# Kernel tuning notes

Hardware: AMD Instinct MI355X
Metric: run time of the kernel (lower is better)

The kernel has to match this reference:

```python
import jax, jax.numpy as jnp
import numpy as np

N_NODES = 51200      # 128 graphs * 400 ROIs
N_ROI = 400
HID = 64             # 'batch_size' arg of the torch module = hidden channels = n_timepoints
N_EDGES = 1638400    # avg degree 32
N_CLASSES = 2
NEG_SLOPE = 0.01


def setup_inputs():
    key = jax.random.key(0)
    ks = jax.random.split(key, 20)
    s = 0.05
    inp = {
        'x': jax.random.normal(ks[0], (N_NODES, HID), dtype=jnp.float32),
        'edge_index': jax.random.randint(ks[1], (2, N_EDGES), 0, N_NODES, dtype=jnp.int64),
        'edge_weight': jax.random.uniform(ks[2], (N_EDGES,), dtype=jnp.float32),
        # GCNConv weights stored [in, out]; biases [out]
        'W1': jax.random.normal(ks[3], (HID, HID), dtype=jnp.float32) * s,
        'b1': jnp.zeros((HID,), jnp.float32),
        'W2': jax.random.normal(ks[4], (HID, HID), dtype=jnp.float32) * s,
        'b2': jnp.zeros((HID,), jnp.float32),
        'W3': jax.random.normal(ks[5], (HID, HID), dtype=jnp.float32) * s,
        'b3': jnp.zeros((HID,), jnp.float32),
        'W4': jax.random.normal(ks[6], (HID, HID), dtype=jnp.float32) * s,
        'b4': jnp.zeros((HID,), jnp.float32),
        'fc1_w': jax.random.normal(ks[7], (N_ROI * HID, 256), dtype=jnp.float32) * 0.01,
        'fc1_b': jnp.zeros((256,), jnp.float32),
        'fc2_w': jax.random.normal(ks[8], (256, 128), dtype=jnp.float32) * s,
        'fc2_b': jnp.zeros((128,), jnp.float32),
        'fc3_w': jax.random.normal(ks[9], (128, N_CLASSES), dtype=jnp.float32) * s,
        'fc3_b': jnp.zeros((N_CLASSES,), jnp.float32),
    }
    return inp


def _gcn_norm(edge_index, edge_weight, n):
    # PyG GCNConv: add self-loops (weight 1), symmetric D^-1/2 A D^-1/2 normalization
    loop = jnp.arange(n, dtype=edge_index.dtype)
    src = jnp.concatenate([edge_index[0], loop])
    dst = jnp.concatenate([edge_index[1], loop])
    w = jnp.concatenate([edge_weight, jnp.ones((n,), edge_weight.dtype)])
    deg = jax.ops.segment_sum(w, dst, num_segments=n)
    dis = jnp.where(deg > 0, jax.lax.rsqrt(jnp.maximum(deg, 1e-30)), 0.0)
    norm = dis[src] * w * dis[dst]
    return src, dst, norm


def _conv(h, W, b, src, dst, norm, n):
    h = h @ W                                   # [N, out]
    msg = h[src] * norm[:, None]                # gather + scale
    out = jax.ops.segment_sum(msg, dst, num_segments=n) + b
    return out


def _leaky(v):
    return jnp.where(v >= 0, v, NEG_SLOPE * v)


def _head(h, fc1_w, fc1_b, fc2_w, fc2_b, fc3_w, fc3_b):
    # global_mean_pool with batch = arange(N) is identity; pool == reshape to graphs
    g = h.reshape(-1, N_ROI * HID)              # [G, n_roi*hid]
    g = g @ fc1_w + fc1_b                       # dropout is eval-mode identity
    g = g @ fc2_w + fc2_b
    g = g @ fc3_w + fc3_b
    return g


def reference(x, edge_index, edge_weight, W1, b1, W2, b2, W3, b3, W4, b4,
              fc1_w, fc1_b, fc2_w, fc2_b, fc3_w, fc3_b):
    n = x.shape[0]
    src, dst, norm = _gcn_norm(edge_index, edge_weight, n)
    h = _leaky(_conv(x, W1, b1, src, dst, norm, n))
    h = _leaky(_conv(h, W2, b2, src, dst, norm, n))
    h = _leaky(_conv(h, W3, b3, src, dst, norm, n))
    h = _leaky(_conv(h, W4, b4, src, dst, norm, n))
    logits = _head(h, fc1_w, fc1_b, fc2_w, fc2_b, fc3_w, fc3_b)
    logits0 = _head(x, fc1_w, fc1_b, fc2_w, fc2_b, fc3_w, fc3_b)
    penal = 0.09 * logits.shape[0] / jnp.linalg.norm(logits - logits0)
    return logits, penal
```

## Files before the change

### kernel.cpp

```cpp
#include <hip/hip_runtime.h>
#include <cstddef>

#define N_NODES 51200
#define N_EDGES 1638400
#define HID 64
#define N_ROI 400
#define N_GRAPHS 128
#define KHEAD 25600
#define NEG_SLOPE 0.01f
#define CAP 80
#define NCHUNK 200
#define CHUNK 8192
#define NBIN 1024
#define BINSZ 50
#define LSTRIDE 81
#define NWC 400

typedef unsigned short u16;
typedef unsigned int u32;
typedef unsigned char u8;
typedef float f32x2 __attribute__((ext_vector_type(2)));

__device__ inline u16 f2bf(float f) {
    u32 u = __float_as_uint(f);
    u32 r = u + 0x7FFFu + ((u >> 16) & 1u);
    return (u16)(r >> 16);
}
__device__ inline float bf2f(u16 h) { return __uint_as_float(((u32)h) << 16); }

__device__ inline f32x2 dec8lo(u32 v) { return __builtin_amdgcn_cvt_pk_f32_fp8((int)v, false); }
__device__ inline f32x2 dec8hi(u32 v) { return __builtin_amdgcn_cvt_pk_f32_fp8((int)v, true); }
template <bool HI>
__device__ inline u32 enc8(float a, float b, u32 old) {
    return (u32)__builtin_amdgcn_cvt_pk_fp8_f32(a, b, (int)old, HI);
}
__device__ inline u32 pack4_fp8(float a, float b, float c, float d) {
    u32 w = enc8<false>(a, b, 0u);
    return enc8<true>(c, d, w);
}


__global__ __launch_bounds__(1024) void k1(const int* __restrict__ ei,
                                           const float* __restrict__ ew,
                                           uint2* __restrict__ chunkData,
                                           u32* __restrict__ offcnt,
                                           const float* __restrict__ x,
                                           u8* __restrict__ x8,
                                           const float* __restrict__ fc2w,
                                           const float* __restrict__ fc3w,
                                           const float* __restrict__ fc1b,
                                           const float* __restrict__ fc2b,
                                           const float* __restrict__ fc3b,
                                           float* __restrict__ fc23,
                                           float* __restrict__ bc,
                                           float* __restrict__ sq,
                                           int* __restrict__ done) {
    int bid = blockIdx.x, t = threadIdx.x;
    __shared__ u32 cnt[NBIN];
    __shared__ u32 cur[NBIN];
    __shared__ u32 wsum[16];
    __shared__ uint2 stag[CHUNK];
    __shared__ float t1[128];

    if (bid < NCHUNK) {
        cnt[t] = 0;
        __syncthreads();
        int base = bid * CHUNK;
        const int4* sp = reinterpret_cast<const int4*>(ei + base);
        const int4* dp = reinterpret_cast<const int4*>(ei + N_EDGES + base);
        const float4* wp = reinterpret_cast<const float4*>(ew + base);
        int4 sa = sp[2 * t], sb = sp[2 * t + 1];
        int4 da = dp[2 * t], db = dp[2 * t + 1];
        float4 wa = wp[2 * t], wb = wp[2 * t + 1];
        int ss[8] = {sa.x, sa.y, sa.z, sa.w, sb.x, sb.y, sb.z, sb.w};
        int dd[8] = {da.x, da.y, da.z, da.w, db.x, db.y, db.z, db.w};
        float wv[8] = {wa.x, wa.y, wa.z, wa.w, wb.x, wb.y, wb.z, wb.w};
        u32 lo[8]; int bin[8];
        #pragma unroll
        for (int i = 0; i < 8; i++) {
            int b = (int)((u32)dd[i] / BINSZ);
            bin[i] = b;
            lo[i] = (u32)ss[i] | ((u32)(dd[i] - b * BINSZ) << 16);
            atomicAdd(&cnt[b], 1u);
        }
        __syncthreads();
        int wave = t >> 6, lane = t & 63;
        u32 v = cnt[t], inc = v;
        #pragma unroll
        for (int d = 1; d < 64; d <<= 1) {
            u32 o = __shfl_up(inc, d, 64);
            if (lane >= d) inc += o;
        }
        if (lane == 63) wsum[wave] = inc;
        __syncthreads();
        if (t == 0) {
            u32 r = 0;
            #pragma unroll
            for (int i = 0; i < 16; i++) { u32 c = wsum[i]; wsum[i] = r; r += c; }
        }
        __syncthreads();
        u32 excl = inc - v + wsum[wave];
        cur[t] = excl;
        offcnt[(size_t)bid * NBIN + t] = excl | (v << 16);
        __syncthreads();
        #pragma unroll
        for (int i = 0; i < 8; i++) {
            u32 pos = atomicAdd(&cur[bin[i]], 1u);
            stag[pos] = make_uint2(lo[i], __float_as_uint(wv[i]));
        }
        __syncthreads();
        const uint4* sg4 = reinterpret_cast<const uint4*>(stag);
        uint4* out4 = reinterpret_cast<uint4*>(chunkData + (size_t)base);
        #pragma unroll
        for (int i = 0; i < 4; i++) out4[i * 1024 + t] = sg4[i * 1024 + t];
    } else if (bid < 400) {
        int idx = (bid - NCHUNK) * 1024 + t;
        const float4* xp = reinterpret_cast<const float4*>(x) + (size_t)idx * 4;
        float4 a = xp[0], b = xp[1], c = xp[2], d = xp[3];
        reinterpret_cast<uint4*>(x8)[idx] =
            make_uint4(pack4_fp8(a.x, a.y, a.z, a.w), pack4_fp8(b.x, b.y, b.z, b.w),
                       pack4_fp8(c.x, c.y, c.z, c.w), pack4_fp8(d.x, d.y, d.z, d.w));
    } else {
        if (t == 256) *sq = 0.f;
        if (t == 257) *done = 0;
        if (t < 256) {
            float s0 = 0.f, s1 = 0.f;
            const float* row = fc2w + t * 128;
            for (int j = 0; j < 128; j++) {
                float a = row[j];
                s0 += a * fc3w[2 * j];
                s1 += a * fc3w[2 * j + 1];
            }
            fc23[2 * t] = s0;
            fc23[2 * t + 1] = s1;
        }
        if (t < 128) {
            float s = fc2b[t];
            for (int k = 0; k < 256; k++) s += fc1b[k] * fc2w[k * 128 + t];
            t1[t] = s;
        }
        __syncthreads();
        if (t < 2) {
            float s = fc3b[t];
            for (int j = 0; j < 128; j++) s += t1[j] * fc3w[2 * j + t];
            bc[t] = s;
        }
    }
}


__global__ __launch_bounds__(256) void k1t(const u32* __restrict__ in,
                                           u32* __restrict__ outT) {
    __shared__ u32 tile[32][33];
    int bx = blockIdx.x & 31, cy = blockIdx.x >> 5;
    int b0 = bx * 32, c0 = cy * 32;
    int tx = threadIdx.x & 31, ty = threadIdx.x >> 5;
    for (int i = ty; i < 32; i += 8) {
        int c = c0 + i;
        if (c < NCHUNK) tile[i][tx] = in[(size_t)c * NBIN + b0 + tx];
    }
    __syncthreads();
    for (int i = ty; i < 32; i += 8) {
        int b = b0 + i;
        int c = c0 + tx;
        if (c < NCHUNK) outT[(size_t)b * NCHUNK + c] = tile[tx][i];
    }
}


__global__ __launch_bounds__(512) void k2(const uint2* __restrict__ chunkData,
                                          const u32* __restrict__ offcntT,
                                          u32* __restrict__ buck,
                                          int* __restrict__ cnts,
                                          float* __restrict__ dis,
                                          const float* __restrict__ fc1w,
                                          const float* __restrict__ fc23,
                                          float* __restrict__ Wc) {
    int bid = blockIdx.x, t = threadIdx.x;
    __shared__ u32 lbuck[BINSZ * LSTRIDE];
    __shared__ u32 lcnt[BINSZ];
    __shared__ float ldeg[BINSZ];
    __shared__ u32 oc[NCHUNK];

    if (bid < NBIN) {
        if (t < BINSZ) { lcnt[t] = 0; ldeg[t] = 0.f; }
        if (t < NCHUNK) oc[t] = offcntT[(size_t)bid * NCHUNK + t];
        __syncthreads();
        int w = t >> 6, lane = t & 63;
        int sBase = w * 25;
        for (int j = 0; j < 32; j += 8) {
            int so = j + (lane >> 3);
            int s = sBase + so;
            int i0 = lane & 7;
            int k = 0, off = 0;
            if (so < 25) {
                u32 o = oc[s];
                off = (int)(o & 0xffffu);
                k = (int)(o >> 16);
            }
            const uint2* cd = chunkData + (size_t)s * CHUNK + off;
            for (int i = i0; i < k; i += 8) {
                uint2 e = cd[i];
                u32 node = e.x >> 16;
                u32 src = e.x & 0xffffu;
                float ww = __uint_as_float(e.y);
                u32 pos = atomicAdd(&lcnt[node], 1u);
                if (pos < CAP - 1) lbuck[node * LSTRIDE + pos] = ((u32)f2bf(ww) << 16) | src;
                atomicAdd(&ldeg[node], ww);
            }
        }
        __syncthreads();
        int sg = t >> 5, ln = t & 31;
        for (int n = sg; n < BINSZ; n += 16) {
            int node = bid * BINSZ + n;
            int k = min((int)lcnt[n], CAP - 1);
            u32* dst = buck + (size_t)node * CAP;
            for (int i = ln; i < k; i += 32) dst[i] = lbuck[n * LSTRIDE + i];
            if (ln == 0) {
                float d = rsqrtf(1.f + ldeg[n]);
                dis[node] = d;
                cnts[node] = k + 1;
                dst[k] = ((u32)f2bf(d * d) << 16) | (u32)node;
            }
        }
    } else {
        float* f23 = (float*)lbuck;
        f23[t] = fc23[t];
        __syncthreads();
        const float2* f2p = reinterpret_cast<const float2*>(f23);
        int row = (bid - NBIN) * 64 + (t >> 3);
        int p = t & 7;
        const float4* rp = reinterpret_cast<const float4*>(fc1w + (size_t)row * 256 + p * 32);
        float s0 = 0.f, s1 = 0.f;
        #pragma unroll
        for (int i = 0; i < 8; i++) {
            float4 a = rp[i];
            int kb = p * 32 + i * 4;
            float2 w0 = f2p[kb], w1 = f2p[kb + 1], w2 = f2p[kb + 2], w3 = f2p[kb + 3];
            s0 += a.x * w0.x + a.y * w1.x + a.z * w2.x + a.w * w3.x;
            s1 += a.x * w0.y + a.y * w1.y + a.z * w2.y + a.w * w3.y;
        }
        #pragma unroll
        for (int off = 4; off; off >>= 1) {
            s0 += __shfl_down(s0, off, 8);
            s1 += __shfl_down(s1, off, 8);
        }
        if (p == 0) reinterpret_cast<float2*>(Wc)[row] = make_float2(s0, s1);
    }
}


template <bool BAKE>
__global__ __launch_bounds__(256) void k_layer(const u8* __restrict__ H8,
                                               u32* __restrict__ buck,
                                               const int* __restrict__ cnts,
                                               const float* __restrict__ dis,
                                               const float* __restrict__ W,
                                               const float* __restrict__ bias,
                                               u8* __restrict__ Hout) {
    __shared__ float Ws[64][64];
    __shared__ float ZsT[64][33];
    int t = threadIdx.x;
    int base = blockIdx.x * 32;

    #pragma unroll
    for (int i = 0; i < 4; i++) {
        int f = t + i * 256;
        int kk = f >> 4, c4 = f & 15;
        float4 wv = reinterpret_cast<const float4*>(W)[f];
        *reinterpret_cast<float4*>(&Ws[kk][c4 * 4]) = wv;
    }

    int grp = t >> 3, sub = t & 7;
    int node = base + grp;
    int k = cnts[node];
    u32* bk = buck + (size_t)node * CAP;

    if (BAKE) {
        float d = dis[node];
        for (int j = sub; j < k - 1; j += 8) {
            u32 e = bk[j];
            float val = bf2f((u16)(e >> 16)) * d * dis[e & 0xffffu];
            bk[j] = ((u32)f2bf(val) << 16) | (e & 0xffffu);
        }
    }

    const uint2* H64 = reinterpret_cast<const uint2*>(H8);
    float a0 = 0.f, a1 = 0.f, a2 = 0.f, a3 = 0.f;
    float a4 = 0.f, a5 = 0.f, a6 = 0.f, a7 = 0.f;
    for (int j0 = 0; j0 < k; j0 += 8) {
        int idx = j0 + sub;
        u32 pre = (idx < k) ? bk[idx] : 0u;
        #pragma unroll
        for (int i = 0; i < 8; i++) {
            u32 e = (u32)__shfl((int)pre, i, 8);
            float val = __uint_as_float(e & 0xffff0000u);
            u32 src = e & 0xffffu;
            uint2 r = H64[(size_t)src * 8 + sub];
            f32x2 l0 = dec8lo(r.x), h0 = dec8hi(r.x);
            f32x2 l1 = dec8lo(r.y), h1 = dec8hi(r.y);
            a0 += val * l0.x; a1 += val * l0.y; a2 += val * h0.x; a3 += val * h0.y;
            a4 += val * l1.x; a5 += val * l1.y; a6 += val * h1.x; a7 += val * h1.y;
        }
    }
    ZsT[8 * sub + 0][grp] = a0; ZsT[8 * sub + 1][grp] = a1;
    ZsT[8 * sub + 2][grp] = a2; ZsT[8 * sub + 3][grp] = a3;
    ZsT[8 * sub + 4][grp] = a4; ZsT[8 * sub + 5][grp] = a5;
    ZsT[8 * sub + 6][grp] = a6; ZsT[8 * sub + 7][grp] = a7;
    __syncthreads();

    int rp2 = t >> 4, c4i = t & 15;
    int r0 = rp2 * 2, c0 = c4i * 4;
    float4 acc0 = {0,0,0,0}, acc1 = {0,0,0,0};
    #pragma unroll 8
    for (int kk = 0; kk < 64; kk++) {
        float z0 = ZsT[kk][r0];
        float z1 = ZsT[kk][r0 + 1];
        float4 w = *reinterpret_cast<const float4*>(&Ws[kk][c0]);
        acc0.x += z0 * w.x; acc0.y += z0 * w.y; acc0.z += z0 * w.z; acc0.w += z0 * w.w;
        acc1.x += z1 * w.x; acc1.y += z1 * w.y; acc1.z += z1 * w.z; acc1.w += z1 * w.w;
    }
    float4 bb = *reinterpret_cast<const float4*>(bias + c0);
    float v0 = acc0.x + bb.x, v1 = acc0.y + bb.y, v2 = acc0.z + bb.z, v3 = acc0.w + bb.w;
    float v4 = acc1.x + bb.x, v5 = acc1.y + bb.y, v6 = acc1.z + bb.z, v7 = acc1.w + bb.w;
    v0 = v0 >= 0.f ? v0 : NEG_SLOPE * v0;
    v1 = v1 >= 0.f ? v1 : NEG_SLOPE * v1;
    v2 = v2 >= 0.f ? v2 : NEG_SLOPE * v2;
    v3 = v3 >= 0.f ? v3 : NEG_SLOPE * v3;
    v4 = v4 >= 0.f ? v4 : NEG_SLOPE * v4;
    v5 = v5 >= 0.f ? v5 : NEG_SLOPE * v5;
    v6 = v6 >= 0.f ? v6 : NEG_SLOPE * v6;
    v7 = v7 >= 0.f ? v7 : NEG_SLOPE * v7;
    u32* outp = reinterpret_cast<u32*>(Hout);
    outp[(size_t)(base + r0) * 16 + c4i]     = pack4_fp8(v0, v1, v2, v3);
    outp[(size_t)(base + r0 + 1) * 16 + c4i] = pack4_fp8(v4, v5, v6, v7);
}


__global__ __launch_bounds__(256) void k_logits(const u8* __restrict__ h4,
                                                const u8* __restrict__ x8,
                                                const float* __restrict__ Wc,
                                                const float* __restrict__ bc,
                                                float* __restrict__ out,
                                                float* __restrict__ sq,
                                                int* __restrict__ done) {
    int g = blockIdx.x, t = threadIdx.x;
    const u8* bh = h4 + (size_t)g * KHEAD;
    const u8* bx = x8 + (size_t)g * KHEAD;
    float aH0 = 0.f, aH1 = 0.f, aX0 = 0.f, aX1 = 0.f;
    for (int k2 = t; k2 < KHEAD / 2; k2 += 256) {
        u32 hv = reinterpret_cast<const u16*>(bh)[k2];
        u32 xv = reinterpret_cast<const u16*>(bx)[k2];
        f32x2 h = dec8lo(hv);
        f32x2 xf = dec8lo(xv);
        float4 wc = reinterpret_cast<const float4*>(Wc)[k2];
        aH0 += h.x * wc.x + h.y * wc.z;
        aH1 += h.x * wc.y + h.y * wc.w;
        aX0 += xf.x * wc.x + xf.y * wc.z;
        aX1 += xf.x * wc.y + xf.y * wc.w;
    }
    for (int off = 32; off > 0; off >>= 1) {
        aH0 += __shfl_down(aH0, off);
        aH1 += __shfl_down(aH1, off);
        aX0 += __shfl_down(aX0, off);
        aX1 += __shfl_down(aX1, off);
    }
    __shared__ float red[4][4];
    int wave = t >> 6, lane = t & 63;
    if (lane == 0) {
        red[wave][0] = aH0; red[wave][1] = aH1;
        red[wave][2] = aX0; red[wave][3] = aX1;
    }
    __syncthreads();
    if (t == 0) {
        float h0 = red[0][0] + red[1][0] + red[2][0] + red[3][0];
        float h1 = red[0][1] + red[1][1] + red[2][1] + red[3][1];
        float x0 = red[0][2] + red[1][2] + red[2][2] + red[3][2];
        float x1 = red[0][3] + red[1][3] + red[2][3] + red[3][3];
        out[2 * g]     = h0 + bc[0];
        out[2 * g + 1] = h1 + bc[1];
        float d0 = h0 - x0, d1 = h1 - x1;
        atomicAdd(sq, d0 * d0 + d1 * d1);
        __threadfence();
        int c = atomicAdd(done, 1);
        if (c == N_GRAPHS - 1) {
            __threadfence();
            float s = atomicAdd(sq, 0.f);
            out[2 * N_GRAPHS] = 0.09f * (float)N_GRAPHS / sqrtf(s);
        }
    }
}


extern "C" void kernel_launch(void* const* d_in, const int* in_sizes, int n_in,
                              void* d_out, int out_size, void* d_ws, size_t ws_size,
                              hipStream_t stream) {
    const float* x    = (const float*)d_in[0];
    const int*   ei   = (const int*)d_in[1];
    const float* ew   = (const float*)d_in[2];
    const float* W1   = (const float*)d_in[3];
    const float* b1   = (const float*)d_in[4];
    const float* W2   = (const float*)d_in[5];
    const float* b2   = (const float*)d_in[6];
    const float* W3   = (const float*)d_in[7];
    const float* b3   = (const float*)d_in[8];
    const float* W4   = (const float*)d_in[9];
    const float* b4   = (const float*)d_in[10];
    const float* fc1w = (const float*)d_in[11];
    const float* fc1b = (const float*)d_in[12];
    const float* fc2w = (const float*)d_in[13];
    const float* fc2b = (const float*)d_in[14];
    const float* fc3w = (const float*)d_in[15];
    const float* fc3b = (const float*)d_in[16];
    float* out = (float*)d_out;

    char* base = (char*)d_ws;
    size_t off = 0;
    auto alloc = [&](size_t bytes) -> void* {
        void* p = base + off;
        off += (bytes + 255) & ~(size_t)255;
        return p;
    };
    uint2* chunkData = (uint2*)alloc((size_t)N_EDGES * 8);
    u32*   offcnt    = (u32*)alloc((size_t)NCHUNK * NBIN * 4);
    u32*   offcntT   = (u32*)alloc((size_t)NCHUNK * NBIN * 4);
    u32*   buck      = (u32*)alloc((size_t)N_NODES * CAP * 4);
    int*   cnts      = (int*)alloc((size_t)N_NODES * 4);
    float* dis       = (float*)alloc((size_t)N_NODES * 4);
    u8*    x8        = (u8*)alloc((size_t)N_NODES * HID);
    u8*    ha        = (u8*)alloc((size_t)N_NODES * HID);
    u8*    hb        = (u8*)alloc((size_t)N_NODES * HID);
    float* fc23      = (float*)alloc(512 * 4);
    float* bc        = (float*)alloc(2 * 4);
    float* Wc        = (float*)alloc((size_t)KHEAD * 2 * 4);
    char*  ctrl      = (char*)alloc(256);
    float* sq        = (float*)ctrl;
    int*   done      = (int*)(ctrl + 4);

    k1<<<401, 1024, 0, stream>>>(ei, ew, chunkData, offcnt, x, x8,
                                 fc2w, fc3w, fc1b, fc2b, fc3b, fc23, bc, sq, done);
    k1t<<<224, 256, 0, stream>>>(offcnt, offcntT);
    k2<<<NBIN + NWC, 512, 0, stream>>>(chunkData, offcntT, buck, cnts, dis,
                                       fc1w, fc23, Wc);

    const float* Wl[4] = {W1, W2, W3, W4};
    const float* bl[4] = {b1, b2, b3, b4};
    u8* hbufs[2] = {ha, hb};
    const u8* hin = x8;
    for (int l = 0; l < 4; l++) {
        u8* hout = hbufs[l & 1];
        if (l == 0)
            k_layer<true><<<N_NODES / 32, 256, 0, stream>>>(hin, buck, cnts, dis,
                                                            Wl[l], bl[l], hout);
        else
            k_layer<false><<<N_NODES / 32, 256, 0, stream>>>(hin, buck, cnts, dis,
                                                             Wl[l], bl[l], hout);
        hin = hout;
    }

    k_logits<<<N_GRAPHS, 256, 0, stream>>>(hin, x8, Wc, bc, out, sq, done);
}
```

Before: 163.8 us.

## Fuse logits head into last GCN layer and overlap x-logits with layer two

Removes the separate k_logits launch. The last layer now multiplies its leaky outputs directly by the collapsed head weights Wc and accumulates per-graph logits with atomics, so the final fp8 activation buffer is never stored or reread. A last-block-done counter finishes the output and the penalty norm. The x-side head dot products run as extra blocks appended to the layer-2 grid. This adds float atomics on per-graph accumulators, a second graph split inside blocks that straddle graphs, and a nondeterministic summation order.

```diff
diff --git a/kernel.cpp b/kernel.cpp
--- a/kernel.cpp
+++ b/kernel.cpp
@@ -15,6 +15,7 @@
 #define BINSZ 50
 #define LSTRIDE 81
 #define NWC 400
+#define NLB (N_NODES / 32)
 
 typedef unsigned short u16;
 typedef unsigned int u32;
@@ -53,7 +54,7 @@
                                            const float* __restrict__ fc3b,
                                            float* __restrict__ fc23,
                                            float* __restrict__ bc,
-                                           float* __restrict__ sq,
+                                           float* __restrict__ glog,
                                            int* __restrict__ done) {
     int bid = blockIdx.x, t = threadIdx.x;
     __shared__ u32 cnt[NBIN];
@@ -121,8 +122,8 @@
             make_uint4(pack4_fp8(a.x, a.y, a.z, a.w), pack4_fp8(b.x, b.y, b.z, b.w),
                        pack4_fp8(c.x, c.y, c.z, c.w), pack4_fp8(d.x, d.y, d.z, d.w));
     } else {
-        if (t == 256) *sq = 0.f;
-        if (t == 257) *done = 0;
+        if (t >= 256 && t < 512) glog[t - 256] = 0.f;
+        if (t == 512) *done = 0;
         if (t < 256) {
             float s0 = 0.f, s1 = 0.f;
             const float* row = fc2w + t * 128;
@@ -250,18 +251,54 @@
 }
 
 
-template <bool BAKE>
+template <bool BAKE, bool EXTRA, bool LAST>
 __global__ __launch_bounds__(256) void k_layer(const u8* __restrict__ H8,
                                                u32* __restrict__ buck,
                                                const int* __restrict__ cnts,
                                                const float* __restrict__ dis,
                                                const float* __restrict__ W,
                                                const float* __restrict__ bias,
-                                               u8* __restrict__ Hout) {
+                                               u8* __restrict__ Hout,
+                                               const u8* __restrict__ x8,
+                                               const float* __restrict__ Wc,
+                                               const float* __restrict__ bc,
+                                               float* __restrict__ glog,
+                                               float* __restrict__ xl,
+                                               float* __restrict__ out,
+                                               int* __restrict__ done) {
     __shared__ float Ws[64][64];
     __shared__ float ZsT[64][33];
+    __shared__ float red[4][4];
+    __shared__ int lastFlag;
     int t = threadIdx.x;
-    int base = blockIdx.x * 32;
+    int bid = blockIdx.x;
+
+    if (EXTRA && bid >= NLB) {
+        int g = bid - NLB;
+        const u16* bx = reinterpret_cast<const u16*>(x8 + (size_t)g * KHEAD);
+        float aX0 = 0.f, aX1 = 0.f;
+        for (int q = t; q < KHEAD / 2; q += 256) {
+            f32x2 xf = dec8lo((u32)bx[q]);
+            float4 wc = reinterpret_cast<const float4*>(Wc)[q];
+            aX0 += xf.x * wc.x + xf.y * wc.z;
+            aX1 += xf.x * wc.y + xf.y * wc.w;
+        }
+        #pragma unroll
+        for (int off = 32; off > 0; off >>= 1) {
+            aX0 += __shfl_down(aX0, off);
+            aX1 += __shfl_down(aX1, off);
+        }
+        int wave = t >> 6, lane = t & 63;
+        if (lane == 0) { red[wave][0] = aX0; red[wave][1] = aX1; }
+        __syncthreads();
+        if (t == 0) {
+            xl[2 * g]     = red[0][0] + red[1][0] + red[2][0] + red[3][0];
+            xl[2 * g + 1] = red[0][1] + red[1][1] + red[2][1] + red[3][1];
+        }
+        return;
+    }
+
+    int base = bid * 32;
 
     #pragma unroll
     for (int i = 0; i < 4; i++) {
@@ -331,62 +368,76 @@
     v5 = v5 >= 0.f ? v5 : NEG_SLOPE * v5;
     v6 = v6 >= 0.f ? v6 : NEG_SLOPE * v6;
     v7 = v7 >= 0.f ? v7 : NEG_SLOPE * v7;
-    u32* outp = reinterpret_cast<u32*>(Hout);
-    outp[(size_t)(base + r0) * 16 + c4i]     = pack4_fp8(v0, v1, v2, v3);
-    outp[(size_t)(base + r0 + 1) * 16 + c4i] = pack4_fp8(v4, v5, v6, v7);
-}
-
-
-__global__ __launch_bounds__(256) void k_logits(const u8* __restrict__ h4,
-                                                const u8* __restrict__ x8,
-                                                const float* __restrict__ Wc,
-                                                const float* __restrict__ bc,
-                                                float* __restrict__ out,
-                                                float* __restrict__ sq,
-                                                int* __restrict__ done) {
-    int g = blockIdx.x, t = threadIdx.x;
-    const u8* bh = h4 + (size_t)g * KHEAD;
-    const u8* bx = x8 + (size_t)g * KHEAD;
-    float aH0 = 0.f, aH1 = 0.f, aX0 = 0.f, aX1 = 0.f;
-    for (int k2 = t; k2 < KHEAD / 2; k2 += 256) {
-        u32 hv = reinterpret_cast<const u16*>(bh)[k2];
-        u32 xv = reinterpret_cast<const u16*>(bx)[k2];
-        f32x2 h = dec8lo(hv);
-        f32x2 xf = dec8lo(xv);
-        float4 wc = reinterpret_cast<const float4*>(Wc)[k2];
-        aH0 += h.x * wc.x + h.y * wc.z;
-        aH1 += h.x * wc.y + h.y * wc.w;
-        aX0 += xf.x * wc.x + xf.y * wc.z;
-        aX1 += xf.x * wc.y + xf.y * wc.w;
-    }
-    for (int off = 32; off > 0; off >>= 1) {
-        aH0 += __shfl_down(aH0, off);
-        aH1 += __shfl_down(aH1, off);
-        aX0 += __shfl_down(aX0, off);
-        aX1 += __shfl_down(aX1, off);
-    }
-    __shared__ float red[4][4];
-    int wave = t >> 6, lane = t & 63;
-    if (lane == 0) {
-        red[wave][0] = aH0; red[wave][1] = aH1;
-        red[wave][2] = aX0; red[wave][3] = aX1;
-    }
-    __syncthreads();
-    if (t == 0) {
-        float h0 = red[0][0] + red[1][0] + red[2][0] + red[3][0];
-        float h1 = red[0][1] + red[1][1] + red[2][1] + red[3][1];
-        float x0 = red[0][2] + red[1][2] + red[2][2] + red[3][2];
-        float x1 = red[0][3] + red[1][3] + red[2][3] + red[3][3];
-        out[2 * g]     = h0 + bc[0];
-        out[2 * g + 1] = h1 + bc[1];
-        float d0 = h0 - x0, d1 = h1 - x1;
-        atomicAdd(sq, d0 * d0 + d1 * d1);
-        __threadfence();
-        int c = atomicAdd(done, 1);
-        if (c == N_GRAPHS - 1) {
+
+    if (!LAST) {
+        u32* outp = reinterpret_cast<u32*>(Hout);
+        outp[(size_t)(base + r0) * 16 + c4i]     = pack4_fp8(v0, v1, v2, v3);
+        outp[(size_t)(base + r0 + 1) * 16 + c4i] = pack4_fp8(v4, v5, v6, v7);
+    } else {
+        int nodeA = base + r0, nodeB = nodeA + 1;
+        int gA = nodeA / N_ROI, gB = nodeB / N_ROI;
+        int roiA = nodeA - gA * N_ROI, roiB = nodeB - gB * N_ROI;
+        const float2* wcp = reinterpret_cast<const float2*>(Wc);
+        float2 wa0 = wcp[roiA * 64 + c0],     wa1 = wcp[roiA * 64 + c0 + 1];
+        float2 wa2 = wcp[roiA * 64 + c0 + 2], wa3 = wcp[roiA * 64 + c0 + 3];
+        float2 wb0 = wcp[roiB * 64 + c0],     wb1 = wcp[roiB * 64 + c0 + 1];
+        float2 wb2 = wcp[roiB * 64 + c0 + 2], wb3 = wcp[roiB * 64 + c0 + 3];
+        float pA0 = v0 * wa0.x + v1 * wa1.x + v2 * wa2.x + v3 * wa3.x;
+        float pA1 = v0 * wa0.y + v1 * wa1.y + v2 * wa2.y + v3 * wa3.y;
+        float pB0 = v4 * wb0.x + v5 * wb1.x + v6 * wb2.x + v7 * wb3.x;
+        float pB1 = v4 * wb0.y + v5 * wb1.y + v6 * wb2.y + v7 * wb3.y;
+        int g0 = base / N_ROI;
+        float q00 = (gA == g0 ? pA0 : 0.f) + (gB == g0 ? pB0 : 0.f);
+        float q01 = (gA == g0 ? pA1 : 0.f) + (gB == g0 ? pB1 : 0.f);
+        float q10 = (gA != g0 ? pA0 : 0.f) + (gB != g0 ? pB0 : 0.f);
+        float q11 = (gA != g0 ? pA1 : 0.f) + (gB != g0 ? pB1 : 0.f);
+        #pragma unroll
+        for (int off = 32; off > 0; off >>= 1) {
+            q00 += __shfl_down(q00, off);
+            q01 += __shfl_down(q01, off);
+            q10 += __shfl_down(q10, off);
+            q11 += __shfl_down(q11, off);
+        }
+        int wave = t >> 6, lane = t & 63;
+        if (lane == 0) {
+            red[wave][0] = q00; red[wave][1] = q01;
+            red[wave][2] = q10; red[wave][3] = q11;
+        }
+        __syncthreads();
+        if (t == 0) {
+            float s00 = red[0][0] + red[1][0] + red[2][0] + red[3][0];
+            float s01 = red[0][1] + red[1][1] + red[2][1] + red[3][1];
+            float s10 = red[0][2] + red[1][2] + red[2][2] + red[3][2];
+            float s11 = red[0][3] + red[1][3] + red[2][3] + red[3][3];
+            atomicAdd(&glog[2 * g0], s00);
+            atomicAdd(&glog[2 * g0 + 1], s01);
+            if (g0 + 1 < N_GRAPHS && (s10 != 0.f || s11 != 0.f)) {
+                atomicAdd(&glog[2 * (g0 + 1)], s10);
+                atomicAdd(&glog[2 * (g0 + 1) + 1], s11);
+            }
             __threadfence();
-            float s = atomicAdd(sq, 0.f);
-            out[2 * N_GRAPHS] = 0.09f * (float)N_GRAPHS / sqrtf(s);
+            lastFlag = (atomicAdd(done, 1) == NLB - 1);
+        }
+        __syncthreads();
+        if (lastFlag) {
+            __threadfence();
+            float part = 0.f;
+            if (t < N_GRAPHS) {
+                float l0 = glog[2 * t], l1 = glog[2 * t + 1];
+                out[2 * t]     = l0 + bc[0];
+                out[2 * t + 1] = l1 + bc[1];
+                float d0 = l0 - xl[2 * t], d1 = l1 - xl[2 * t + 1];
+                part = d0 * d0 + d1 * d1;
+            }
+            #pragma unroll
+            for (int off = 32; off > 0; off >>= 1) part += __shfl_down(part, off);
+            int wave2 = t >> 6, lane2 = t & 63;
+            if (lane2 == 0) red[wave2][0] = part;
+            __syncthreads();
+            if (t == 0) {
+                float s = red[0][0] + red[1][0] + red[2][0] + red[3][0];
+                out[2 * N_GRAPHS] = 0.09f * (float)N_GRAPHS / sqrtf(s);
+            }
         }
     }
 }
@@ -433,30 +484,24 @@
     float* fc23      = (float*)alloc(512 * 4);
     float* bc        = (float*)alloc(2 * 4);
     float* Wc        = (float*)alloc((size_t)KHEAD * 2 * 4);
+    float* glog      = (float*)alloc(256 * 4);
+    float* xl        = (float*)alloc(256 * 4);
     char*  ctrl      = (char*)alloc(256);
-    float* sq        = (float*)ctrl;
-    int*   done      = (int*)(ctrl + 4);
+    int*   done      = (int*)ctrl;
 
     k1<<<401, 1024, 0, stream>>>(ei, ew, chunkData, offcnt, x, x8,
-                                 fc2w, fc3w, fc1b, fc2b, fc3b, fc23, bc, sq, done);
+                                 fc2w, fc3w, fc1b, fc2b, fc3b, fc23, bc,
+                                 glog, done);
     k1t<<<224, 256, 0, stream>>>(offcnt, offcntT);
     k2<<<NBIN + NWC, 512, 0, stream>>>(chunkData, offcntT, buck, cnts, dis,
                                        fc1w, fc23, Wc);
 
-    const float* Wl[4] = {W1, W2, W3, W4};
-    const float* bl[4] = {b1, b2, b3, b4};
-    u8* hbufs[2] = {ha, hb};
-    const u8* hin = x8;
-    for (int l = 0; l < 4; l++) {
-        u8* hout = hbufs[l & 1];
-        if (l == 0)
-            k_layer<true><<<N_NODES / 32, 256, 0, stream>>>(hin, buck, cnts, dis,
-                                                            Wl[l], bl[l], hout);
-        else
-            k_layer<false><<<N_NODES / 32, 256, 0, stream>>>(hin, buck, cnts, dis,
-                                                             Wl[l], bl[l], hout);
-        hin = hout;
-    }
-
-    k_logits<<<N_GRAPHS, 256, 0, stream>>>(hin, x8, Wc, bc, out, sq, done);
-}
+    k_layer<true, false, false><<<NLB, 256, 0, stream>>>(
+        x8, buck, cnts, dis, W1, b1, ha, x8, Wc, bc, glog, xl, out, done);
+    k_layer<false, true, false><<<NLB + N_GRAPHS, 256, 0, stream>>>(
+        ha, buck, cnts, dis, W2, b2, hb, x8, Wc, bc, glog, xl, out, done);
+    k_layer<false, false, false><<<NLB, 256, 0, stream>>>(
+        hb, buck, cnts, dis, W3, b3, ha, x8, Wc, bc, glog, xl, out, done);
+    k_layer<false, false, true><<<NLB, 256, 0, stream>>>(
+        ha, buck, cnts, dis, W4, b4, hb, x8, Wc, bc, glog, xl, out, done);
+}
```

New measurement: 185.0 us. +13.0%, slower.
